# Kernel optimization log

Hardware: AMD Instinct MI355X
Metric: run time of the kernel (lower is better)

Reference implementation:

```python
import jax, jax.numpy as jnp
import numpy as np

B, N, D, H, DM = 4, 1024, 1024, 16, 4096
DH = D // H
SCALE = DH ** -0.5
EPS = 1e-5


def layer_norm(x, g, b):
    mu = jnp.mean(x, axis=-1, keepdims=True)
    var = jnp.mean((x - mu) ** 2, axis=-1, keepdims=True)
    return (x - mu) * jax.lax.rsqrt(var + EPS) * g + b


def mha(q_in, k_in, v_in, Wq, bq, Wk, bk, Wv, bv, Wp, bp):
    # weights stored (in, out); torch Linear equivalent y = x @ W + b
    q = (q_in @ Wq + bq).reshape(B, -1, H, DH).transpose(0, 2, 1, 3)  # (B,H,Nq,DH)
    k = (k_in @ Wk + bk).reshape(B, -1, H, DH).transpose(0, 2, 1, 3)
    v = (v_in @ Wv + bv).reshape(B, -1, H, DH).transpose(0, 2, 1, 3)
    attn = jax.nn.softmax(jnp.einsum('bhqd,bhkd->bhqk', q, k) * SCALE, axis=-1)
    x = jnp.einsum('bhqk,bhkd->bhqd', attn, v).transpose(0, 2, 1, 3).reshape(B, -1, D)
    return x @ Wp + bp


def setup_inputs() -> dict:
    key = jax.random.key(0)
    ks = jax.random.split(key, 32)
    s = 0.02
    inp = {
        'tokens_enc': jax.random.normal(ks[0], (B, N, D), jnp.float32),
        'tokens_dec': jax.random.normal(ks[1], (B, N, D), jnp.float32),
        'PE_enc': jax.random.normal(ks[2], (B, N, D), jnp.float32),
        'PE_dec': jax.random.normal(ks[3], (B, N, D), jnp.float32),
    }
    names = ['sa_Wq', 'sa_Wk', 'sa_Wv', 'sa_Wp', 'ca_Wq', 'ca_Wk', 'ca_Wv', 'ca_Wp']
    for i, n in enumerate(names):
        inp[n] = jax.random.normal(ks[4 + i], (D, D), jnp.float32) * s
        inp[n.replace('W', 'b')] = jnp.zeros((D,), jnp.float32)
    inp['mlp_W1'] = jax.random.normal(ks[12], (D, DM), jnp.float32) * s
    inp['mlp_b1'] = jnp.zeros((DM,), jnp.float32)
    inp['mlp_W2'] = jax.random.normal(ks[13], (DM, D), jnp.float32) * s
    inp['mlp_b2'] = jnp.zeros((D,), jnp.float32)
    for i in (1, 2, 3):
        inp[f'ln{i}_g'] = jnp.ones((D,), jnp.float32)
        inp[f'ln{i}_b'] = jnp.zeros((D,), jnp.float32)
    return inp


def reference(tokens_enc, tokens_dec, PE_enc, PE_dec,
              sa_Wq, sa_bq, sa_Wk, sa_bk, sa_Wv, sa_bv, sa_Wp, sa_bp,
              ca_Wq, ca_bq, ca_Wk, ca_bk, ca_Wv, ca_bv, ca_Wp, ca_bp,
              mlp_W1, mlp_b1, mlp_W2, mlp_b2,
              ln1_g, ln1_b, ln2_g, ln2_b, ln3_g, ln3_b):
    # SA (pre-norm): q=k=ln(x)+PE_dec, v=ln(x)
    x2 = layer_norm(tokens_dec, ln1_g, ln1_b)
    qk = x2 + PE_dec
    tokens_dec = tokens_dec + mha(qk, qk, x2, sa_Wq, sa_bq, sa_Wk, sa_bk, sa_Wv, sa_bv, sa_Wp, sa_bp)
    # CA: q=ln(x)+PE_dec, k=enc+PE_enc, v=enc
    x2 = layer_norm(tokens_dec, ln2_g, ln2_b)
    tokens_dec = tokens_dec + mha(x2 + PE_dec, tokens_enc + PE_enc, tokens_enc,
                                  ca_Wq, ca_bq, ca_Wk, ca_bk, ca_Wv, ca_bv, ca_Wp, ca_bp)
    # FFD
    x2 = layer_norm(tokens_dec, ln3_g, ln3_b)
    h = jax.nn.gelu(x2 @ mlp_W1 + mlp_b1, approximate=False)
    return tokens_dec + (h @ mlp_W2 + mlp_b2)
```

## Files before the change

### kernel.cpp

```cpp
#include <hip/hip_runtime.h>
#include <hip/hip_bf16.h>
#include <math.h>

#define B_ 4
#define N_ 1024
#define D_ 1024
#define H_ 16
#define DH_ 64
#define DM_ 4096
#define NT_ (B_*N_)
#define EPS_ 1e-5f
#define SCALE_ 0.125f
#define CEXP_ 0.1803368801111244f

typedef unsigned short u16;
typedef short s16x8 __attribute__((ext_vector_type(8)));
typedef __bf16 y16x8 __attribute__((ext_vector_type(8)));
typedef float f32x4 __attribute__((ext_vector_type(4)));
typedef float f32x16 __attribute__((ext_vector_type(16)));

#define ZERO16 (f32x16){0.f,0.f,0.f,0.f,0.f,0.f,0.f,0.f,0.f,0.f,0.f,0.f,0.f,0.f,0.f,0.f}

__device__ __forceinline__ u16 f2bs(float f) {
  unsigned int u = __builtin_bit_cast(unsigned int, f);
  u += 0x7fffu + ((u >> 16) & 1u);
  return (u16)(u >> 16);
}

static __device__ __forceinline__ f32x4 MFMA(y16x8 a, y16x8 b, f32x4 c) {
  return __builtin_amdgcn_mfma_f32_16x16x32_bf16(a, b, c, 0, 0, 0);
}
static __device__ __forceinline__ f32x16 MFMA32(y16x8 a, y16x8 b, f32x16 c) {
  return __builtin_amdgcn_mfma_f32_32x32x16_bf16(a, b, c, 0, 0, 0);
}

static __device__ __forceinline__ unsigned cvtpk(float a, float b) {
  unsigned r;
  asm("v_cvt_pk_bf16_f32 %0, %1, %2" : "=v"(r) : "v"(a), "v"(b));
  return r;
}

static __device__ __forceinline__ void async16(void* lds, const void* g) {
  __builtin_amdgcn_global_load_lds(
      (const __attribute__((address_space(1))) unsigned int*)g,
      (__attribute__((address_space(3))) unsigned int*)lds, 16, 0, 0);
}

__global__ __launch_bounds__(256) void k_wtrans8(
    const float* __restrict__ s0, const float* __restrict__ s1,
    const float* __restrict__ s2, const float* __restrict__ s3,
    const float* __restrict__ s4, const float* __restrict__ s5,
    const float* __restrict__ s6, const float* __restrict__ s7,
    u16* __restrict__ dst) {
  const float* srcs[8] = {s0, s1, s2, s3, s4, s5, s6, s7};
  const float* W = srcs[blockIdx.z];
  u16* Wt = dst + (size_t)blockIdx.z * D_ * D_;
  __shared__ u16 tile[32][33];
  int n0 = blockIdx.x * 32, k0 = blockIdx.y * 32;
  int tx = threadIdx.x & 31, ty = threadIdx.x >> 5;
#pragma unroll
  for (int i = 0; i < 4; ++i) {
    int k = k0 + ty + i * 8;
    tile[ty + i * 8][tx] = f2bs(W[(size_t)k * D_ + n0 + tx]);
  }
  __syncthreads();
#pragma unroll
  for (int i = 0; i < 4; ++i) {
    int n = n0 + ty + i * 8;
    Wt[(size_t)n * D_ + k0 + tx] = tile[tx][ty + i * 8];
  }
}

__global__ __launch_bounds__(256) void k_wtrans(const float* __restrict__ W,
                                                u16* __restrict__ Wt,
                                                int K, int Ncols) {
  __shared__ u16 tile[32][33];
  int n0 = blockIdx.x * 32, k0 = blockIdx.y * 32;
  int tx = threadIdx.x & 31, ty = threadIdx.x >> 5;
#pragma unroll
  for (int i = 0; i < 4; ++i) {
    int k = k0 + ty + i * 8;
    tile[ty + i * 8][tx] = f2bs(W[(size_t)k * Ncols + n0 + tx]);
  }
  __syncthreads();
#pragma unroll
  for (int i = 0; i < 4; ++i) {
    int n = n0 + ty + i * 8;
    Wt[(size_t)n * K + k0 + tx] = tile[tx][ty + i * 8];
  }
}

__global__ __launch_bounds__(256) void k_encprep(const float* __restrict__ enc,
                                                 const float* __restrict__ pe,
                                                 u16* __restrict__ encpe,
                                                 u16* __restrict__ encv) {
  int i = blockIdx.x * 256 + threadIdx.x;
  float4 e = ((const float4*)enc)[i];
  float4 p = ((const float4*)pe)[i];
  union { u16 u[4]; uint2 v; } a, b;
  a.u[0] = f2bs(e.x + p.x); a.u[1] = f2bs(e.y + p.y);
  a.u[2] = f2bs(e.z + p.z); a.u[3] = f2bs(e.w + p.w);
  b.u[0] = f2bs(e.x); b.u[1] = f2bs(e.y); b.u[2] = f2bs(e.z); b.u[3] = f2bs(e.w);
  ((uint2*)encpe)[i] = a.v;
  ((uint2*)encv)[i] = b.v;
}

__global__ __launch_bounds__(256) void k_ln(const float* __restrict__ x,
                                            const float* __restrict__ g,
                                            const float* __restrict__ bta,
                                            const float* __restrict__ pe,
                                            u16* __restrict__ x2o,
                                            u16* __restrict__ qko) {
  int row = blockIdx.x;
  int t = threadIdx.x;
  float4 v = ((const float4*)(x + (size_t)row * D_))[t];
  float s = v.x + v.y + v.z + v.w;
#pragma unroll
  for (int o = 1; o < 64; o <<= 1) s += __shfl_xor(s, o, 64);
  __shared__ float red[8];
  if ((t & 63) == 0) red[t >> 6] = s;
  __syncthreads();
  float mean = (red[0] + red[1] + red[2] + red[3]) * (1.0f / D_);
  float dx = v.x - mean, dy = v.y - mean, dz = v.z - mean, dw = v.w - mean;
  float s2 = dx * dx + dy * dy + dz * dz + dw * dw;
#pragma unroll
  for (int o = 1; o < 64; o <<= 1) s2 += __shfl_xor(s2, o, 64);
  if ((t & 63) == 0) red[4 + (t >> 6)] = s2;
  __syncthreads();
  float var = (red[4] + red[5] + red[6] + red[7]) * (1.0f / D_);
  float rstd = rsqrtf(var + EPS_);
  float4 gv = ((const float4*)g)[t];
  float4 bv = ((const float4*)bta)[t];
  float y0 = dx * rstd * gv.x + bv.x;
  float y1 = dy * rstd * gv.y + bv.y;
  float y2 = dz * rstd * gv.z + bv.z;
  float y3 = dw * rstd * gv.w + bv.w;
  union { u16 u[4]; uint2 v2; } o1;
  o1.u[0] = f2bs(y0); o1.u[1] = f2bs(y1); o1.u[2] = f2bs(y2); o1.u[3] = f2bs(y3);
  ((uint2*)(x2o + (size_t)row * D_))[t] = o1.v2;
  if (pe) {
    float4 pv = ((const float4*)(pe + (size_t)row * D_))[t];
    union { u16 u[4]; uint2 v2; } o2;
    o2.u[0] = f2bs(y0 + pv.x); o2.u[1] = f2bs(y1 + pv.y);
    o2.u[2] = f2bs(y2 + pv.z); o2.u[3] = f2bs(y3 + pv.w);
    ((uint2*)(qko + (size_t)row * D_))[t] = o2.v2;
  }
}

template <int EPI>
__global__ __launch_bounds__(256) void k_gemm(const u16* __restrict__ A,
                                              const u16* __restrict__ Bt,
                                              const float* __restrict__ bias,
                                              const float* __restrict__ res,
                                              float* __restrict__ outf,
                                              u16* __restrict__ outb,
                                              int M, int Nn, int K, int ldo) {
  constexpr int BM = 128, BN = 128, BK = 64;
  __shared__ __align__(128) char smem[2][(BM + BN) * BK * 2];
  const int t = threadIdx.x;
  const int wave = t >> 6, lane = t & 63, lg = lane >> 4, lc = lane & 15;
  const int nwg = gridDim.x * gridDim.y;
  const int bid = blockIdx.y * gridDim.x + blockIdx.x;
  const int lb = (bid & 7) * (nwg >> 3) + (bid >> 3);
  const int bx = lb % gridDim.x, by = lb / gridDim.x;
  const int m0 = by * BM, n0 = bx * BN;
  const int wm = (wave >> 1) * 64, wn = (wave & 1) * 64;
  f32x4 acc[4][4];
#pragma unroll
  for (int i = 0; i < 4; ++i)
#pragma unroll
    for (int j = 0; j < 4; ++j) acc[i][j] = (f32x4){0.f, 0.f, 0.f, 0.f};
  const char* Ag = (const char*)(A + (size_t)m0 * K);
  const char* Bg = (const char*)(Bt + (size_t)n0 * K);
  const int sr = t >> 3, sp = t & 7;

  auto stage = [&](int bufi, int kt) {
    char* sA = smem[bufi];
    char* sB = smem[bufi] + BM * BK * 2;
#pragma unroll
    for (int rr = 0; rr < 4; ++rr) {
      int row = rr * 32 + sr;
      int c = sp ^ (row & 7);
      async16(sA + (size_t)row * 128 + sp * 16,
              Ag + ((size_t)row * K + kt + c * 8) * 2);
      async16(sB + (size_t)row * 128 + sp * 16,
              Bg + ((size_t)row * K + kt + c * 8) * 2);
    }
  };
  auto compute = [&](int bufi) {
    const char* sA = smem[bufi];
    const char* sB = smem[bufi] + BM * BK * 2;
#pragma unroll
    for (int ks = 0; ks < 2; ++ks) {
      y16x8 af[4], bfr[4];
#pragma unroll
      for (int fm = 0; fm < 4; ++fm) {
        int R = wm + fm * 16 + lc;
        int pc = (ks * 4 + lg) ^ (R & 7);
        af[fm] = *(const y16x8*)(sA + (size_t)R * 128 + pc * 16);
      }
#pragma unroll
      for (int fn = 0; fn < 4; ++fn) {
        int R = wn + fn * 16 + lc;
        int pc = (ks * 4 + lg) ^ (R & 7);
        bfr[fn] = *(const y16x8*)(sB + (size_t)R * 128 + pc * 16);
      }
#pragma unroll
      for (int fm = 0; fm < 4; ++fm)
#pragma unroll
        for (int fn = 0; fn < 4; ++fn)
          acc[fm][fn] = MFMA(af[fm], bfr[fn], acc[fm][fn]);
    }
  };

  stage(0, 0);
  __syncthreads();
  int cur = 0;
  for (int kt = BK; kt < K; kt += BK) {
    stage(cur ^ 1, kt);
    compute(cur);
    __syncthreads();
    cur ^= 1;
  }
  compute(cur);

#pragma unroll
  for (int fm = 0; fm < 4; ++fm)
#pragma unroll
    for (int fn = 0; fn < 4; ++fn)
#pragma unroll
      for (int j = 0; j < 4; ++j) {
        int row = m0 + wm + fm * 16 + lg * 4 + j;
        int col = n0 + wn + fn * 16 + lc;
        float vv = acc[fm][fn][j] + bias[col];
        size_t idx = (size_t)row * ldo + col;
        if constexpr (EPI == 0) {
          outb[idx] = f2bs(vv);
        } else if constexpr (EPI == 1) {
          outf[idx] = vv + res[idx];
        } else {
          float gx = 0.5f * vv * (1.0f + erff(vv * 0.70710678118f));
          outb[idx] = f2bs(gx);
        }
      }
}

__global__ __launch_bounds__(256) void k_vtrans(const u16* __restrict__ v,
                                                u16* __restrict__ vt) {
  __shared__ u16 tile[32][33];
  int bh = blockIdx.z, b = bh >> 4, h = bh & 15;
  int n0 = blockIdx.x * 32, d0 = blockIdx.y * 32;
  int tx = threadIdx.x & 31, ty = threadIdx.x >> 5;
#pragma unroll
  for (int i = 0; i < 4; ++i) {
    int n = n0 + ty + i * 8;
    tile[ty + i * 8][tx] = v[((size_t)b * N_ + n) * D_ + h * DH_ + d0 + tx];
  }
  __syncthreads();
#pragma unroll
  for (int i = 0; i < 4; ++i) {
    int dh = d0 + ty + i * 8;
    vt[((size_t)bh * DH_ + dh) * N_ + n0 + tx] = tile[tx][ty + i * 8];
  }
}

__global__ __launch_bounds__(256) void k_attn(const u16* __restrict__ q, int qs,
                                              const u16* __restrict__ k, int ks2,
                                              const u16* __restrict__ vt,
                                              u16* __restrict__ out) {
  __shared__ __align__(16) u16 Kl[64][64];
  __shared__ __align__(16) u16 Vl[64][64];
  __shared__ __align__(16) u16 Ol[4][32][72];
  const int lb = blockIdx.x;
  const int bh = (lb & 7) | ((lb >> 6) << 3);
  const int qb = (lb >> 3) & 7;
  const int b = bh >> 4, h = bh & 15;
  const int t = threadIdx.x, wave = t >> 6, lane = t & 63;
  const int ql = lane & 31, hi = lane >> 5;
  const int q0 = qb * 128 + wave * 32;
  const u16* qp = q + ((size_t)b * N_ + q0) * qs + h * DH_;
  const u16* kp = k + (size_t)b * N_ * ks2 + h * DH_;
  const u16* vp = vt + ((size_t)bh * DH_) * N_;

  y16x8 aq[4];
#pragma unroll
  for (int s = 0; s < 4; ++s)
    aq[s] = *(const y16x8*)(qp + (size_t)ql * qs + s * 16 + hi * 8);

  f32x16 o0 = ZERO16, o1 = ZERO16;
  float m_r = -1e30f, l_r = 0.f;

  for (int kt = 0; kt < N_; kt += 64) {
    __syncthreads();
#pragma unroll
    for (int rr = 0; rr < 2; ++rr) {
      int id = rr * 256 + t;
      int row = id >> 3, c = id & 7;
      int pc2 = c ^ (row & 7);
      *(s16x8*)&Kl[row][pc2 * 8] =
          *(const s16x8*)(kp + (size_t)(kt + row) * ks2 + c * 8);
      *(s16x8*)&Vl[row][pc2 * 8] =
          *(const s16x8*)(vp + (size_t)row * N_ + kt + c * 8);
    }
    __syncthreads();

    f32x16 st0 = ZERO16, st1 = ZERO16;
#pragma unroll
    for (int s = 0; s < 4; ++s) {
      int pc0 = ((s * 2 + hi) ^ (ql & 7)) * 8;
      y16x8 ak0 = *(const y16x8*)&Kl[ql][pc0];
      y16x8 ak1 = *(const y16x8*)&Kl[32 + ql][pc0];
      st0 = MFMA32(ak0, aq[s], st0);
      st1 = MFMA32(ak1, aq[s], st1);
    }

    float mx = st0[0];
#pragma unroll
    for (int r = 1; r < 16; ++r) mx = fmaxf(mx, st0[r]);
#pragma unroll
    for (int r = 0; r < 16; ++r) mx = fmaxf(mx, st1[r]);
    mx = fmaxf(mx, __shfl_xor(mx, 32, 64));
    float mn = fmaxf(m_r, mx);
    float corr = exp2f((m_r - mn) * CEXP_);
    float ps = 0.f;
#pragma unroll
    for (int r = 0; r < 16; ++r) {
      float e = exp2f((st0[r] - mn) * CEXP_); st0[r] = e; ps += e;
    }
#pragma unroll
    for (int r = 0; r < 16; ++r) {
      float e = exp2f((st1[r] - mn) * CEXP_); st1[r] = e; ps += e;
    }
    ps += __shfl_xor(ps, 32, 64);
    l_r = l_r * corr + ps;
    m_r = mn;
    o0 = o0 * corr;
    o1 = o1 * corr;

#pragma unroll
    for (int ks = 0; ks < 4; ++ks) {
      unsigned A0, A1, B0, B1;
      if (ks < 2) {
        const int il = ks * 8;
        A0 = cvtpk(st0[il + 0], st0[il + 1]);
        A1 = cvtpk(st0[il + 2], st0[il + 3]);
        B0 = cvtpk(st0[il + 4], st0[il + 5]);
        B1 = cvtpk(st0[il + 6], st0[il + 7]);
      } else {
        const int il = (ks - 2) * 8;
        A0 = cvtpk(st1[il + 0], st1[il + 1]);
        A1 = cvtpk(st1[il + 2], st1[il + 3]);
        B0 = cvtpk(st1[il + 4], st1[il + 5]);
        B1 = cvtpk(st1[il + 6], st1[il + 7]);
      }
      asm("v_permlane32_swap_b32 %0, %1" : "+v"(A0), "+v"(B0));
      asm("v_permlane32_swap_b32 %0, %1" : "+v"(A1), "+v"(B1));
      union { unsigned w[4]; y16x8 v; } fr;
      fr.w[0] = A0; fr.w[1] = A1; fr.w[2] = B0; fr.w[3] = B1;
      int pc = ((ks * 2 + hi) ^ (ql & 7)) * 8;
      y16x8 bv0 = *(const y16x8*)&Vl[ql][pc];
      y16x8 bv1 = *(const y16x8*)&Vl[32 + ql][pc];
      o0 = MFMA32(bv0, fr.v, o0);
      o1 = MFMA32(bv1, fr.v, o1);
    }
  }

  float rl = 1.f / l_r;
#pragma unroll
  for (int rq = 0; rq < 4; ++rq)
#pragma unroll
    for (int e = 0; e < 4; e += 2) {
      *(unsigned*)&Ol[wave][ql][8 * rq + 4 * hi + e] =
          cvtpk(o0[rq * 4 + e] * rl, o0[rq * 4 + e + 1] * rl);
      *(unsigned*)&Ol[wave][ql][32 + 8 * rq + 4 * hi + e] =
          cvtpk(o1[rq * 4 + e] * rl, o1[rq * 4 + e + 1] * rl);
    }
#pragma unroll
  for (int pp = 0; pp < 4; ++pp) {
    int row = pp * 8 + (lane >> 3);
    s16x8 vv = *(const s16x8*)&Ol[wave][row][(lane & 7) * 8];
    *(s16x8*)(out + ((size_t)b * N_ + q0 + row) * D_ + h * DH_ + (lane & 7) * 8) = vv;
  }
}

extern "C" void kernel_launch(void* const* d_in, const int* in_sizes, int n_in,
                              void* d_out, int out_size, void* d_ws, size_t ws_size,
                              hipStream_t stream) {
  const float* tokens_enc = (const float*)d_in[0];
  const float* tokens_dec = (const float*)d_in[1];
  const float* PE_enc = (const float*)d_in[2];
  const float* PE_dec = (const float*)d_in[3];
  const float* sa_Wq = (const float*)d_in[4];  const float* sa_bq = (const float*)d_in[5];
  const float* sa_Wk = (const float*)d_in[6];  const float* sa_bk = (const float*)d_in[7];
  const float* sa_Wv = (const float*)d_in[8];  const float* sa_bv = (const float*)d_in[9];
  const float* sa_Wp = (const float*)d_in[10]; const float* sa_bp = (const float*)d_in[11];
  const float* ca_Wq = (const float*)d_in[12]; const float* ca_bq = (const float*)d_in[13];
  const float* ca_Wk = (const float*)d_in[14]; const float* ca_bk = (const float*)d_in[15];
  const float* ca_Wv = (const float*)d_in[16]; const float* ca_bv = (const float*)d_in[17];
  const float* ca_Wp = (const float*)d_in[18]; const float* ca_bp = (const float*)d_in[19];
  const float* mlp_W1 = (const float*)d_in[20]; const float* mlp_b1 = (const float*)d_in[21];
  const float* mlp_W2 = (const float*)d_in[22]; const float* mlp_b2 = (const float*)d_in[23];
  const float* ln1_g = (const float*)d_in[24]; const float* ln1_b = (const float*)d_in[25];
  const float* ln2_g = (const float*)d_in[26]; const float* ln2_b = (const float*)d_in[27];
  const float* ln3_g = (const float*)d_in[28]; const float* ln3_b = (const float*)d_in[29];

  char* wsp = (char*)d_ws;
  size_t off = 0;
  auto alloc = [&](size_t bytes) -> char* {
    char* p = wsp + off;
    off += (bytes + 255) & ~(size_t)255;
    return p;
  };
  u16* w8   = (u16*)alloc((size_t)8 * D_ * D_ * 2);
  u16* w1T  = (u16*)alloc((size_t)DM_ * D_ * 2);
  u16* w2T  = (u16*)alloc((size_t)D_ * DM_ * 2);
  float* bqk = (float*)alloc((size_t)2 * D_ * 4);
  u16* encpe = (u16*)alloc((size_t)NT_ * D_ * 2);
  u16* encv  = (u16*)alloc((size_t)NT_ * D_ * 2);
  u16* x2b = (u16*)alloc((size_t)NT_ * D_ * 2);
  u16* qkb = (u16*)alloc((size_t)NT_ * D_ * 2);
  u16* qkm = (u16*)alloc((size_t)NT_ * 2 * D_ * 2);
  u16* vb  = (u16*)alloc((size_t)NT_ * D_ * 2);
  u16* vtb = (u16*)alloc((size_t)NT_ * D_ * 2);
  u16* attb = (u16*)alloc((size_t)NT_ * D_ * 2);
  float* dec1 = (float*)alloc((size_t)NT_ * D_ * 4);
  float* dec2 = (float*)alloc((size_t)NT_ * D_ * 4);
  u16* hb = (u16*)alloc((size_t)NT_ * DM_ * 2);

  const size_t DD = (size_t)D_ * D_;
  u16* wqkT = w8;
  u16* wvT  = w8 + 2 * DD;
  u16* wpT  = w8 + 3 * DD;
  u16* cwqT = w8 + 4 * DD;
  u16* cwkT = w8 + 5 * DD;
  u16* cwvT = w8 + 6 * DD;
  u16* cwpT = w8 + 7 * DD;

  k_wtrans8<<<dim3(32, 32, 8), 256, 0, stream>>>(sa_Wq, sa_Wk, sa_Wv, sa_Wp,
                                                 ca_Wq, ca_Wk, ca_Wv, ca_Wp, w8);
  k_wtrans<<<dim3(128, 32), 256, 0, stream>>>(mlp_W1, w1T, D_, DM_);
  k_wtrans<<<dim3(32, 128), 256, 0, stream>>>(mlp_W2, w2T, DM_, D_);
  hipMemcpyAsync(bqk, sa_bq, D_ * sizeof(float), hipMemcpyDeviceToDevice, stream);
  hipMemcpyAsync(bqk + D_, sa_bk, D_ * sizeof(float), hipMemcpyDeviceToDevice, stream);
  k_encprep<<<dim3(NT_ * D_ / 1024), 256, 0, stream>>>(tokens_enc, PE_enc, encpe, encv);

  k_ln<<<dim3(NT_), 256, 0, stream>>>(tokens_dec, ln1_g, ln1_b, PE_dec, x2b, qkb);
  k_gemm<0><<<dim3(16, 32), 256, 0, stream>>>(qkb, wqkT, bqk, nullptr, nullptr, qkm, NT_, 2 * D_, D_, 2 * D_);
  k_gemm<0><<<dim3(8, 32), 256, 0, stream>>>(x2b, wvT, sa_bv, nullptr, nullptr, vb, NT_, D_, D_, D_);
  k_vtrans<<<dim3(32, 2, 64), 256, 0, stream>>>(vb, vtb);
  k_attn<<<dim3(512), 256, 0, stream>>>(qkm, 2 * D_, qkm + D_, 2 * D_, vtb, attb);
  k_gemm<1><<<dim3(8, 32), 256, 0, stream>>>(attb, wpT, sa_bp, tokens_dec, dec1, nullptr, NT_, D_, D_, D_);

  k_ln<<<dim3(NT_), 256, 0, stream>>>(dec1, ln2_g, ln2_b, PE_dec, x2b, qkb);
  k_gemm<0><<<dim3(8, 32), 256, 0, stream>>>(qkb, cwqT, ca_bq, nullptr, nullptr, qkm, NT_, D_, D_, 2 * D_);
  k_gemm<0><<<dim3(8, 32), 256, 0, stream>>>(encpe, cwkT, ca_bk, nullptr, nullptr, qkm + D_, NT_, D_, D_, 2 * D_);
  k_gemm<0><<<dim3(8, 32), 256, 0, stream>>>(encv, cwvT, ca_bv, nullptr, nullptr, vb, NT_, D_, D_, D_);
  k_vtrans<<<dim3(32, 2, 64), 256, 0, stream>>>(vb, vtb);
  k_attn<<<dim3(512), 256, 0, stream>>>(qkm, 2 * D_, qkm + D_, 2 * D_, vtb, attb);
  k_gemm<1><<<dim3(8, 32), 256, 0, stream>>>(attb, cwpT, ca_bp, dec1, dec2, nullptr, NT_, D_, D_, D_);

  k_ln<<<dim3(NT_), 256, 0, stream>>>(dec2, ln3_g, ln3_b, nullptr, x2b, nullptr);
  k_gemm<2><<<dim3(32, 32), 256, 0, stream>>>(x2b, w1T, mlp_b1, nullptr, nullptr, hb, NT_, DM_, D_, DM_);
  k_gemm<1><<<dim3(8, 32), 256, 0, stream>>>(hb, w2T, mlp_b2, dec2, (float*)d_out, nullptr, NT_, D_, DM_, D_);
}
```

Baseline: 393.3 us.

## Group QKV projections into one launch, fuse V transpose, use 8-wave GEMM tiles

Adds a grouped GEMM kernel that computes the Q, K and V projections in a single launch using blockIdx.z. The V output is written directly in the head-transposed layout, so the separate transpose kernel and its intermediate buffer go away. All GEMMs move from 4 waves to 8 waves per 128x128 tile, with each wave owning a 64x32 sub-tile. This removes launches and extra memory passes and raises wave count, at the cost of less register-level reuse per wave and narrow 8-byte strided stores in the V epilogue.

```diff
diff --git a/kernel.cpp b/kernel.cpp
--- a/kernel.cpp
+++ b/kernel.cpp
@@ -148,7 +148,7 @@
 }
 
 template <int EPI>
-__global__ __launch_bounds__(256) void k_gemm(const u16* __restrict__ A,
+__global__ __launch_bounds__(512) void k_gemm(const u16* __restrict__ A,
                                               const u16* __restrict__ Bt,
                                               const float* __restrict__ bias,
                                               const float* __restrict__ res,
@@ -164,12 +164,12 @@
   const int lb = (bid & 7) * (nwg >> 3) + (bid >> 3);
   const int bx = lb % gridDim.x, by = lb / gridDim.x;
   const int m0 = by * BM, n0 = bx * BN;
-  const int wm = (wave >> 1) * 64, wn = (wave & 1) * 64;
-  f32x4 acc[4][4];
+  const int wm = (wave >> 2) * 64, wn = (wave & 3) * 32;
+  f32x4 acc[4][2];
 #pragma unroll
   for (int i = 0; i < 4; ++i)
 #pragma unroll
-    for (int j = 0; j < 4; ++j) acc[i][j] = (f32x4){0.f, 0.f, 0.f, 0.f};
+    for (int j = 0; j < 2; ++j) acc[i][j] = (f32x4){0.f, 0.f, 0.f, 0.f};
   const char* Ag = (const char*)(A + (size_t)m0 * K);
   const char* Bg = (const char*)(Bt + (size_t)n0 * K);
   const int sr = t >> 3, sp = t & 7;
@@ -178,8 +178,8 @@
     char* sA = smem[bufi];
     char* sB = smem[bufi] + BM * BK * 2;
 #pragma unroll
-    for (int rr = 0; rr < 4; ++rr) {
-      int row = rr * 32 + sr;
+    for (int rr = 0; rr < 2; ++rr) {
+      int row = rr * 64 + sr;
       int c = sp ^ (row & 7);
       async16(sA + (size_t)row * 128 + sp * 16,
               Ag + ((size_t)row * K + kt + c * 8) * 2);
@@ -192,7 +192,7 @@
     const char* sB = smem[bufi] + BM * BK * 2;
 #pragma unroll
     for (int ks = 0; ks < 2; ++ks) {
-      y16x8 af[4], bfr[4];
+      y16x8 af[4], bfr[2];
 #pragma unroll
       for (int fm = 0; fm < 4; ++fm) {
         int R = wm + fm * 16 + lc;
@@ -200,7 +200,7 @@
         af[fm] = *(const y16x8*)(sA + (size_t)R * 128 + pc * 16);
       }
 #pragma unroll
-      for (int fn = 0; fn < 4; ++fn) {
+      for (int fn = 0; fn < 2; ++fn) {
         int R = wn + fn * 16 + lc;
         int pc = (ks * 4 + lg) ^ (R & 7);
         bfr[fn] = *(const y16x8*)(sB + (size_t)R * 128 + pc * 16);
@@ -208,7 +208,7 @@
 #pragma unroll
       for (int fm = 0; fm < 4; ++fm)
 #pragma unroll
-        for (int fn = 0; fn < 4; ++fn)
+        for (int fn = 0; fn < 2; ++fn)
           acc[fm][fn] = MFMA(af[fm], bfr[fn], acc[fm][fn]);
     }
   };
@@ -227,7 +227,7 @@
 #pragma unroll
   for (int fm = 0; fm < 4; ++fm)
 #pragma unroll
-    for (int fn = 0; fn < 4; ++fn)
+    for (int fn = 0; fn < 2; ++fn)
 #pragma unroll
       for (int j = 0; j < 4; ++j) {
         int row = m0 + wm + fm * 16 + lg * 4 + j;
@@ -245,22 +245,113 @@
       }
 }
 
-__global__ __launch_bounds__(256) void k_vtrans(const u16* __restrict__ v,
-                                                u16* __restrict__ vt) {
-  __shared__ u16 tile[32][33];
-  int bh = blockIdx.z, b = bh >> 4, h = bh & 15;
-  int n0 = blockIdx.x * 32, d0 = blockIdx.y * 32;
-  int tx = threadIdx.x & 31, ty = threadIdx.x >> 5;
-#pragma unroll
-  for (int i = 0; i < 4; ++i) {
-    int n = n0 + ty + i * 8;
-    tile[ty + i * 8][tx] = v[((size_t)b * N_ + n) * D_ + h * DH_ + d0 + tx];
-  }
+__global__ __launch_bounds__(512) void k_gemmG(
+    const u16* __restrict__ A0, const u16* __restrict__ A1,
+    const u16* __restrict__ A2, const u16* __restrict__ W0,
+    const u16* __restrict__ W1, const u16* __restrict__ W2,
+    const float* __restrict__ b0, const float* __restrict__ b1,
+    const float* __restrict__ b2, u16* __restrict__ outqk,
+    u16* __restrict__ outvt) {
+  constexpr int BM = 128, BN = 128, BK = 64, K = D_;
+  __shared__ __align__(128) char smem[2][(BM + BN) * BK * 2];
+  const int z = blockIdx.z;
+  const u16* A = z == 0 ? A0 : (z == 1 ? A1 : A2);
+  const u16* Bt = z == 0 ? W0 : (z == 1 ? W1 : W2);
+  const float* bias = z == 0 ? b0 : (z == 1 ? b1 : b2);
+  const int t = threadIdx.x;
+  const int wave = t >> 6, lane = t & 63, lg = lane >> 4, lc = lane & 15;
+  const int nwg = gridDim.x * gridDim.y;
+  const int bid = blockIdx.y * gridDim.x + blockIdx.x;
+  const int lb = (bid & 7) * (nwg >> 3) + (bid >> 3);
+  const int bx = lb % gridDim.x, by = lb / gridDim.x;
+  const int m0 = by * BM, n0 = bx * BN;
+  const int wm = (wave >> 2) * 64, wn = (wave & 3) * 32;
+  f32x4 acc[4][2];
+#pragma unroll
+  for (int i = 0; i < 4; ++i)
+#pragma unroll
+    for (int j = 0; j < 2; ++j) acc[i][j] = (f32x4){0.f, 0.f, 0.f, 0.f};
+  const char* Ag = (const char*)(A + (size_t)m0 * K);
+  const char* Bg = (const char*)(Bt + (size_t)n0 * K);
+  const int sr = t >> 3, sp = t & 7;
+
+  auto stage = [&](int bufi, int kt) {
+    char* sA = smem[bufi];
+    char* sB = smem[bufi] + BM * BK * 2;
+#pragma unroll
+    for (int rr = 0; rr < 2; ++rr) {
+      int row = rr * 64 + sr;
+      int c = sp ^ (row & 7);
+      async16(sA + (size_t)row * 128 + sp * 16,
+              Ag + ((size_t)row * K + kt + c * 8) * 2);
+      async16(sB + (size_t)row * 128 + sp * 16,
+              Bg + ((size_t)row * K + kt + c * 8) * 2);
+    }
+  };
+  auto compute = [&](int bufi) {
+    const char* sA = smem[bufi];
+    const char* sB = smem[bufi] + BM * BK * 2;
+#pragma unroll
+    for (int ks = 0; ks < 2; ++ks) {
+      y16x8 af[4], bfr[2];
+#pragma unroll
+      for (int fm = 0; fm < 4; ++fm) {
+        int R = wm + fm * 16 + lc;
+        int pc = (ks * 4 + lg) ^ (R & 7);
+        af[fm] = *(const y16x8*)(sA + (size_t)R * 128 + pc * 16);
+      }
+#pragma unroll
+      for (int fn = 0; fn < 2; ++fn) {
+        int R = wn + fn * 16 + lc;
+        int pc = (ks * 4 + lg) ^ (R & 7);
+        bfr[fn] = *(const y16x8*)(sB + (size_t)R * 128 + pc * 16);
+      }
+#pragma unroll
+      for (int fm = 0; fm < 4; ++fm)
+#pragma unroll
+        for (int fn = 0; fn < 2; ++fn)
+          acc[fm][fn] = MFMA(af[fm], bfr[fn], acc[fm][fn]);
+    }
+  };
+
+  stage(0, 0);
   __syncthreads();
-#pragma unroll
-  for (int i = 0; i < 4; ++i) {
-    int dh = d0 + ty + i * 8;
-    vt[((size_t)bh * DH_ + dh) * N_ + n0 + tx] = tile[tx][ty + i * 8];
+  int cur = 0;
+  for (int kt = BK; kt < K; kt += BK) {
+    stage(cur ^ 1, kt);
+    compute(cur);
+    __syncthreads();
+    cur ^= 1;
+  }
+  compute(cur);
+
+  if (z < 2) {
+#pragma unroll
+    for (int fm = 0; fm < 4; ++fm)
+#pragma unroll
+      for (int fn = 0; fn < 2; ++fn)
+#pragma unroll
+        for (int j = 0; j < 4; ++j) {
+          int row = m0 + wm + fm * 16 + lg * 4 + j;
+          int col = n0 + wn + fn * 16 + lc;
+          outqk[(size_t)row * (2 * D_) + z * D_ + col] =
+              f2bs(acc[fm][fn][j] + bias[col]);
+        }
+  } else {
+#pragma unroll
+    for (int fm = 0; fm < 4; ++fm)
+#pragma unroll
+      for (int fn = 0; fn < 2; ++fn) {
+        int row0 = m0 + wm + fm * 16 + lg * 4;
+        int col = n0 + wn + fn * 16 + lc;
+        int bb = row0 >> 10, nn = row0 & (N_ - 1);
+        int h = col >> 6, dh = col & 63;
+        float bcol = bias[col];
+        union { u16 u[4]; uint2 v; } pk;
+#pragma unroll
+        for (int j = 0; j < 4; ++j) pk.u[j] = f2bs(acc[fm][fn][j] + bcol);
+        *(uint2*)&outvt[(((size_t)bb * H_ + h) * DH_ + dh) * N_ + nn] = pk.v;
+      }
   }
 }
 
@@ -414,13 +505,11 @@
   u16* w8   = (u16*)alloc((size_t)8 * D_ * D_ * 2);
   u16* w1T  = (u16*)alloc((size_t)DM_ * D_ * 2);
   u16* w2T  = (u16*)alloc((size_t)D_ * DM_ * 2);
-  float* bqk = (float*)alloc((size_t)2 * D_ * 4);
   u16* encpe = (u16*)alloc((size_t)NT_ * D_ * 2);
   u16* encv  = (u16*)alloc((size_t)NT_ * D_ * 2);
   u16* x2b = (u16*)alloc((size_t)NT_ * D_ * 2);
   u16* qkb = (u16*)alloc((size_t)NT_ * D_ * 2);
   u16* qkm = (u16*)alloc((size_t)NT_ * 2 * D_ * 2);
-  u16* vb  = (u16*)alloc((size_t)NT_ * D_ * 2);
   u16* vtb = (u16*)alloc((size_t)NT_ * D_ * 2);
   u16* attb = (u16*)alloc((size_t)NT_ * D_ * 2);
   float* dec1 = (float*)alloc((size_t)NT_ * D_ * 4);
@@ -428,7 +517,8 @@
   u16* hb = (u16*)alloc((size_t)NT_ * DM_ * 2);
 
   const size_t DD = (size_t)D_ * D_;
-  u16* wqkT = w8;
+  u16* wqT  = w8;
+  u16* wkT  = w8 + 1 * DD;
   u16* wvT  = w8 + 2 * DD;
   u16* wpT  = w8 + 3 * DD;
   u16* cwqT = w8 + 4 * DD;
@@ -440,26 +530,21 @@
                                                  ca_Wq, ca_Wk, ca_Wv, ca_Wp, w8);
   k_wtrans<<<dim3(128, 32), 256, 0, stream>>>(mlp_W1, w1T, D_, DM_);
   k_wtrans<<<dim3(32, 128), 256, 0, stream>>>(mlp_W2, w2T, DM_, D_);
-  hipMemcpyAsync(bqk, sa_bq, D_ * sizeof(float), hipMemcpyDeviceToDevice, stream);
-  hipMemcpyAsync(bqk + D_, sa_bk, D_ * sizeof(float), hipMemcpyDeviceToDevice, stream);
   k_encprep<<<dim3(NT_ * D_ / 1024), 256, 0, stream>>>(tokens_enc, PE_enc, encpe, encv);
 
   k_ln<<<dim3(NT_), 256, 0, stream>>>(tokens_dec, ln1_g, ln1_b, PE_dec, x2b, qkb);
-  k_gemm<0><<<dim3(16, 32), 256, 0, stream>>>(qkb, wqkT, bqk, nullptr, nullptr, qkm, NT_, 2 * D_, D_, 2 * D_);
-  k_gemm<0><<<dim3(8, 32), 256, 0, stream>>>(x2b, wvT, sa_bv, nullptr, nullptr, vb, NT_, D_, D_, D_);
-  k_vtrans<<<dim3(32, 2, 64), 256, 0, stream>>>(vb, vtb);
+  k_gemmG<<<dim3(8, 32, 3), 512, 0, stream>>>(qkb, qkb, x2b, wqT, wkT, wvT,
+                                              sa_bq, sa_bk, sa_bv, qkm, vtb);
   k_attn<<<dim3(512), 256, 0, stream>>>(qkm, 2 * D_, qkm + D_, 2 * D_, vtb, attb);
-  k_gemm<1><<<dim3(8, 32), 256, 0, stream>>>(attb, wpT, sa_bp, tokens_dec, dec1, nullptr, NT_, D_, D_, D_);
+  k_gemm<1><<<dim3(8, 32), 512, 0, stream>>>(attb, wpT, sa_bp, tokens_dec, dec1, nullptr, NT_, D_, D_, D_);
 
   k_ln<<<dim3(NT_), 256, 0, stream>>>(dec1, ln2_g, ln2_b, PE_dec, x2b, qkb);
-  k_gemm<0><<<dim3(8, 32), 256, 0, stream>>>(qkb, cwqT, ca_bq, nullptr, nullptr, qkm, NT_, D_, D_, 2 * D_);
-  k_gemm<0><<<dim3(8, 32), 256, 0, stream>>>(encpe, cwkT, ca_bk, nullptr, nullptr, qkm + D_, NT_, D_, D_, 2 * D_);
-  k_gemm<0><<<dim3(8, 32), 256, 0, stream>>>(encv, cwvT, ca_bv, nullptr, nullptr, vb, NT_, D_, D_, D_);
-  k_vtrans<<<dim3(32, 2, 64), 256, 0, stream>>>(vb, vtb);
+  k_gemmG<<<dim3(8, 32, 3), 512, 0, stream>>>(qkb, encpe, encv, cwqT, cwkT, cwvT,
+                                              ca_bq, ca_bk, ca_bv, qkm, vtb);
   k_attn<<<dim3(512), 256, 0, stream>>>(qkm, 2 * D_, qkm + D_, 2 * D_, vtb, attb);
-  k_gemm<1><<<dim3(8, 32), 256, 0, stream>>>(attb, cwpT, ca_bp, dec1, dec2, nullptr, NT_, D_, D_, D_);
+  k_gemm<1><<<dim3(8, 32), 512, 0, stream>>>(attb, cwpT, ca_bp, dec1, dec2, nullptr, NT_, D_, D_, D_);
 
   k_ln<<<dim3(NT_), 256, 0, stream>>>(dec2, ln3_g, ln3_b, nullptr, x2b, nullptr);
-  k_gemm<2><<<dim3(32, 32), 256, 0, stream>>>(x2b, w1T, mlp_b1, nullptr, nullptr, hb, NT_, DM_, D_, DM_);
-  k_gemm<1><<<dim3(8, 32), 256, 0, stream>>>(hb, w2T, mlp_b2, dec2, (float*)d_out, nullptr, NT_, D_, DM_, D_);
-}
+  k_gemm<2><<<dim3(32, 32), 512, 0, stream>>>(x2b, w1T, mlp_b1, nullptr, nullptr, hb, NT_, DM_, D_, DM_);
+  k_gemm<1><<<dim3(8, 32), 512, 0, stream>>>(hb, w2T, mlp_b2, dec2, (float*)d_out, nullptr, NT_, D_, DM_, D_);
+}
```

New measurement: 355.3 us. 9.7% less time.
